# Kernel optimization log

Measured on AMD Instinct MI355X. Metric: run time of the kernel, lower is better.

## Reference

```python
import jax, jax.numpy as jnp
import numpy as np

ALPHA = 2.0      # spikingjelly surrogate.ATan default alpha
TAU_LIF = 2.0    # LIFNode tau
V_TH = 1.0       # spike threshold (v_reset = 0.0, hard reset)


@jax.custom_vjp
def spike_fn(x):
    # Heaviside forward (spikingjelly: x >= 0 -> 1)
    return (x >= 0.0).astype(x.dtype)

def _spike_fwd(x):
    return spike_fn(x), x

def _spike_bwd(x, g):
    # ATan surrogate gradient: alpha/2 / (1 + (pi/2 * alpha * x)^2)
    return (g * (ALPHA / 2.0) / (1.0 + (jnp.pi / 2.0 * ALPHA * x) ** 2),)

spike_fn.defvjp(_spike_fwd, _spike_bwd)


def setup_inputs() -> dict:
    key = jax.random.key(0)
    ks = jax.random.split(key, 5)
    B, T, I, H, O = 256, 1000, 700, 64, 20
    x = jax.random.normal(ks[0], (B, T, I), dtype=jnp.float32)
    W_h = jax.random.normal(ks[1], (H, I), dtype=jnp.float32) / np.sqrt(I).astype(np.float32)
    b_h = jnp.zeros((H,), dtype=jnp.float32)
    W_r = jax.random.normal(ks[2], (O, H), dtype=jnp.float32) / np.sqrt(H).astype(np.float32)
    b_r = jnp.zeros((O,), dtype=jnp.float32)
    tau_m = jax.random.uniform(ks[3], (O,), dtype=jnp.float32, minval=0.0, maxval=4.0)
    return {"x": x, "W_h": W_h, "b_h": b_h, "W_r": W_r, "b_r": b_r, "tau_m": tau_m}


def reference(x, W_h, b_h, W_r, b_r, tau_m):
    B, T, I = x.shape
    H = W_h.shape[0]
    O = W_r.shape[0]
    # One big GEMM for all hidden input currents: [T, B, H]
    currents = jnp.einsum('bti,hi->tbh', x, W_h) + b_h
    beta = jax.nn.sigmoid(tau_m)  # readout leak [O]
    # original accumulates softmax only for t > 10
    mask = (jnp.arange(T) > 10).astype(x.dtype)

    def step(carry, inp):
        v, v_ro, acc = carry
        cur, m = inp
        # LIF charge (decay_input=True, v_reset=0): v += (cur - v)/tau
        v = v + (cur - v) / TAU_LIF
        s = spike_fn(v - V_TH)
        # hard reset to v_reset = 0
        v = v * (1.0 - s)
        # readout leaky integrator
        ro_in = s @ W_r.T + b_r                      # [B, O]
        v_ro = v_ro * beta + (1.0 - beta) * ro_in
        acc = acc + m * jax.nn.softmax(v_ro, axis=-1)
        return (v, v_ro, acc), None

    init = (jnp.zeros((B, H), x.dtype),
            jnp.zeros((B, O), x.dtype),
            jnp.zeros((B, O), x.dtype))
    (_, _, acc), _ = jax.lax.scan(step, init, (currents, mask))
    return acc
```

## Files before the change

kernel.cpp:

```cpp
#include <hip/hip_runtime.h>


typedef float  f32x4  __attribute__((ext_vector_type(4)));
typedef short  short8 __attribute__((ext_vector_type(8)));
typedef unsigned long long ull;

#define B_   256
#define T_   1000
#define K_   700
#define H_   64
#define O_   20
#define NKT  22
#define NCH  200
#define TCH  5
#define TCL  100
#define NCL  10
#define BIL  40

#define OFF_WFRAG  ((size_t)0)
#define OFF_CUR    ((size_t)262144)
#define OFF_MASK   ((size_t)65798144)

__global__ void wprep(const float* __restrict__ Wh, unsigned short* __restrict__ wfrag) {
    int e = blockIdx.x * 256 + threadIdx.x;
    int kt   = e >> 8;
    int rem  = e & 255;
    int nf   = rem >> 6;
    int lane = rem & 63;
    int h     = nf * 16 + (lane & 15);
    int kbase = kt * 32 + ((lane >> 4) & 3) * 8;
    unsigned short* dh = wfrag + (size_t)kt * 4096 + (nf * 64 + lane) * 8;
    unsigned short* dl = dh + 2048;
#pragma unroll
    for (int j = 0; j < 8; ++j) {
        int k = kbase + j;
        float v = (k < K_) ? Wh[(size_t)h * K_ + k] : 0.0f;
        unsigned u  = __builtin_bit_cast(unsigned, v);
        float    fh = __builtin_bit_cast(float, u & 0xffff0000u);
        float    r  = v - fh;
        dh[j] = (unsigned short)(u >> 16);
        dl[j] = (unsigned short)(__builtin_bit_cast(unsigned, r) >> 16);
    }
}

__device__ __forceinline__ void glds16(const void* src, void* lds) {
    __builtin_amdgcn_global_load_lds(
        (const __attribute__((address_space(1))) void*)src,
        (__attribute__((address_space(3))) void*)lds, 16, 0, 0);
}

__device__ __forceinline__ void splitpair(f32x4 p0, f32x4 p1, short8& hi, short8& lo) {
#pragma unroll
    for (int j = 0; j < 4; ++j) {
        {
            unsigned u  = __builtin_bit_cast(unsigned, p0[j]);
            float    fh = __builtin_bit_cast(float, u & 0xffff0000u);
            float    r  = p0[j] - fh;
            hi[j] = (short)(u >> 16);
            lo[j] = (short)(__builtin_bit_cast(unsigned, r) >> 16);
        }
        {
            unsigned u  = __builtin_bit_cast(unsigned, p1[j]);
            float    fh = __builtin_bit_cast(float, u & 0xffff0000u);
            float    r  = p1[j] - fh;
            hi[j + 4] = (short)(u >> 16);
            lo[j + 4] = (short)(__builtin_bit_cast(unsigned, r) >> 16);
        }
    }
}

__device__ __forceinline__ void stage_x32(const float* __restrict__ x, size_t row0,
                                          int kt, int lane, int wid, float* sbuf) {
#pragma unroll
    for (int j = 0; j < 4; ++j) {
        int c   = j * 256 + wid * 64 + lane;
        int row = c >> 3;
        int col = c & 7;
        int csw = (col ^ (row & 7)) << 4;
        int kbyte = kt * 128 + csw;
        if (kbyte + 16 > K_ * 4) kbyte = 0;
        const char* src = (const char*)(x + (row0 + row) * (size_t)K_) + kbyte;
        float* dst = sbuf + (size_t)(j * 256 + wid * 64) * 4;
        glds16(src, dst);
    }
}

__device__ __forceinline__ void stage_w32(const unsigned short* __restrict__ wfrag,
                                          int kt, int lane, int wid, unsigned short* sbuf) {
#pragma unroll
    for (int j = 0; j < 2; ++j) {
        int c = j * 256 + wid * 64 + lane;
        int l = c ^ ((c >> 4) & 7);
        const unsigned short* src = wfrag + (size_t)kt * 4096 + l * 8;
        unsigned short* dst = sbuf + (size_t)(j * 256 + wid * 64) * 8;
        glds16(src, dst);
    }
}

__device__ __forceinline__ void compute32(const float* sbx_, const unsigned short* sbw_,
                                          int lane, int wid, f32x4 (&acc)[2][4]) {
    const f32x4*  xb = (const f32x4*)sbx_;
    const short8* wb = (const short8*)sbw_;
    short8 ah[2], al[2];
    int v0 = (lane >> 4) * 2;
#pragma unroll
    for (int i = 0; i < 2; ++i) {
        int r  = wid * 32 + i * 16 + (lane & 15);
        int c0 = r * 8 + (v0 ^ (r & 7));
        int c1 = r * 8 + ((v0 + 1) ^ (r & 7));
        splitpair(xb[c0], xb[c1], ah[i], al[i]);
    }
#pragma unroll
    for (int n = 0; n < 4; ++n) {
        int lh = n * 64 + lane;
        int ph = lh ^ ((lh >> 4) & 7);
        short8 bhf = wb[ph];
        short8 blf = wb[ph + 256];
#pragma unroll
        for (int i = 0; i < 2; ++i) {
            acc[i][n] = __builtin_amdgcn_mfma_f32_16x16x32_bf16(ah[i], bhf, acc[i][n], 0, 0, 0);
            acc[i][n] = __builtin_amdgcn_mfma_f32_16x16x32_bf16(al[i], bhf, acc[i][n], 0, 0, 0);
            acc[i][n] = __builtin_amdgcn_mfma_f32_16x16x32_bf16(ah[i], blf, acc[i][n], 0, 0, 0);
        }
    }
}

__global__ __launch_bounds__(256, 3) void gemm_cur(const float* __restrict__ x,
                                                   const unsigned short* __restrict__ wfrag,
                                                   const float* __restrict__ b_h,
                                                   float* __restrict__ cur) {
    __shared__ float          sbx[2][4096];
    __shared__ unsigned short sbw[2][4096];
    int tid  = threadIdx.x;
    int lane = tid & 63;
    int wid  = tid >> 6;
    size_t row0 = (size_t)blockIdx.x * 128;

    float bh4[4];
#pragma unroll
    for (int n = 0; n < 4; ++n) bh4[n] = b_h[n * 16 + (lane & 15)];

    f32x4 acc[2][4];
#pragma unroll
    for (int i = 0; i < 2; ++i)
#pragma unroll
        for (int n = 0; n < 4; ++n) acc[i][n] = (f32x4){0.f, 0.f, 0.f, 0.f};

    stage_x32(x, row0, 0, lane, wid, sbx[0]);  stage_w32(wfrag, 0, lane, wid, sbw[0]);
    stage_x32(x, row0, 1, lane, wid, sbx[1]);  stage_w32(wfrag, 1, lane, wid, sbw[1]);

#define GSTEP(T, N)                                                          \
    {                                                                        \
        asm volatile("s_waitcnt vmcnt(" #N ")" ::: "memory");                \
        __builtin_amdgcn_s_barrier();                                        \
        compute32(sbx[(T) & 1], sbw[(T) & 1], lane, wid, acc);               \
        asm volatile("s_waitcnt lgkmcnt(0)" ::: "memory");                   \
        __builtin_amdgcn_s_barrier();                                        \
        if ((T) + 2 < NKT) {                                                 \
            stage_x32(x, row0, (T) + 2, lane, wid, sbx[(T) & 1]);            \
            stage_w32(wfrag, (T) + 2, lane, wid, sbw[(T) & 1]);              \
        }                                                                    \
    }
    GSTEP(0, 6)   GSTEP(1, 6)   GSTEP(2, 6)   GSTEP(3, 6)   GSTEP(4, 6)
    GSTEP(5, 6)   GSTEP(6, 6)   GSTEP(7, 6)   GSTEP(8, 6)   GSTEP(9, 6)
    GSTEP(10, 6)  GSTEP(11, 6)  GSTEP(12, 6)  GSTEP(13, 6)  GSTEP(14, 6)
    GSTEP(15, 6)  GSTEP(16, 6)  GSTEP(17, 6)  GSTEP(18, 6)  GSTEP(19, 6)
    GSTEP(20, 6)  GSTEP(21, 0)
#undef GSTEP

    f32x4* cur4 = (f32x4*)cur;
#pragma unroll
    for (int i = 0; i < 2; ++i) {
        size_t r4 = row0 + wid * 32 + i * 16 + ((lane >> 4) & 3) * 4;
#pragma unroll
        for (int n = 0; n < 4; ++n) {
            f32x4 q;
#pragma unroll
            for (int j = 0; j < 4; ++j) q[j] = acc[i][n][j] + bh4[n];
            cur4[(r4 >> 2) * 64 + n * 16 + (lane & 15)] = q;
        }
    }
}

__global__ __launch_bounds__(64) void lif(const float* __restrict__ cur, ull* __restrict__ masks) {
    int b = blockIdx.x & 255;
    int c = blockIdx.x >> 8;
    int h = threadIdx.x;
    int t0 = c * TCL;
    int ts = (c == 0) ? 0 : (t0 - BIL);
    const f32x4* p = (const f32x4*)cur + (((size_t)b * T_ + ts) >> 2) * 64 + h;
    float v = 0.0f;
    int ngb = (t0 - ts) >> 2;
    for (int g = 0; g < ngb; ++g) {
        f32x4 q = p[g * 64];
#pragma unroll
        for (int j = 0; j < 4; ++j) {
            v = (v + q[j]) * 0.5f;
            v = (v >= 1.0f) ? 0.0f : v;
        }
    }
    p += (size_t)ngb * 64;
    ull* mp = masks + (size_t)b * T_ + t0;
#pragma unroll 2
    for (int g = 0; g < TCL / 4; ++g) {
        f32x4 q = p[g * 64];
#pragma unroll
        for (int j = 0; j < 4; ++j) {
            v = (v + q[j]) * 0.5f;
            bool s = (v >= 1.0f);
            ull m = __ballot(s);
            if (h == 0) mp[g * 4 + j] = m;
            v = s ? 0.0f : v;
        }
    }
}

__global__ __launch_bounds__(512) void readout(const ull* __restrict__ masks,
                                               const float* __restrict__ Wr,
                                               const float* __restrict__ br,
                                               const float* __restrict__ tau,
                                               float* __restrict__ out) {
    __shared__ __align__(16) float wt[64][20];
    __shared__ ull  smask[T_];
    __shared__ __align__(16) float E[NCH][20];
    __shared__ __align__(16) float Sv[NCH][20];
    __shared__ __align__(16) float pacc[NCH][20];
    __shared__ __align__(16) float sScale[20], sBase[20], sBeta[20];
    __shared__ float Pg[8][20], Sst[8][20], part[8][20];

    int tid = threadIdx.x;
    int b   = blockIdx.x;
    for (int i = tid; i < 1280; i += 512) wt[i & 63][i >> 6] = Wr[(size_t)(i >> 6) * 64 + (i & 63)];
    for (int i = tid; i < T_; i += 512) smask[i] = masks[(size_t)b * T_ + i];
    if (tid < 20) {
        float beta = 1.0f / (1.0f + __expf(-tau[tid]));
        sBeta[tid]  = beta;
        sScale[tid] = 1.0f - beta;
        sBase[tid]  = br[tid];
    }
    __syncthreads();

    for (int it = tid; it < NCH * 5; it += 512) {
        int o4 = it % 5;
        int c  = it / 5;
        f32x4 beta4  = *(const f32x4*)&sBeta[o4 * 4];
        f32x4 scale4 = *(const f32x4*)&sScale[o4 * 4];
        f32x4 base4  = *(const f32x4*)&sBase[o4 * 4];
        f32x4 v = {0.f, 0.f, 0.f, 0.f};
        const ull* mp = smask + c * TCH;
#pragma unroll
        for (int j = 0; j < TCH; ++j) {
            ull m = mp[j];
            f32x4 a = {0.f, 0.f, 0.f, 0.f};
            while (m) {
                int h = __builtin_ctzll(m);
                m &= (m - 1);
                a += *(const f32x4*)&wt[h][o4 * 4];
            }
            f32x4 q;
#pragma unroll
            for (int jj = 0; jj < 4; ++jj) q[jj] = scale4[jj] * (base4[jj] + a[jj]);
            v = beta4 * v + q;
        }
        *(f32x4*)&E[c][o4 * 4] = v;
    }
    __syncthreads();

    if (tid < 160) {
        int o = tid >> 3, g = tid & 7;
        float beta = sBeta[o];
        float b2 = beta * beta;
        float bp = b2 * b2 * beta;
        float P = 0.0f;
        for (int c = g * 25; c < g * 25 + 25; ++c) P = bp * P + E[c][o];
        Pg[g][o] = P;
    }
    __syncthreads();

    if (tid < 20) {
        int o = tid;
        float beta = sBeta[o];
        float b2 = beta * beta;
        float bp = b2 * b2 * beta;
        float bp25 = 1.0f;
#pragma unroll
        for (int i = 0; i < 25; ++i) bp25 *= bp;
        float s = 0.0f;
        for (int g = 0; g < 8; ++g) { Sst[g][o] = s; s = bp25 * s + Pg[g][o]; }
    }
    __syncthreads();

    if (tid < 160) {
        int o = tid >> 3, g = tid & 7;
        float beta = sBeta[o];
        float b2 = beta * beta;
        float bp = b2 * b2 * beta;
        float s = Sst[g][o];
        for (int c = g * 25; c < g * 25 + 25; ++c) { Sv[c][o] = s; s = bp * s + E[c][o]; }
    }
    __syncthreads();

    if (tid < NCH) {
        int c = tid;
        float beta[20], v[20], acc[20];
#pragma unroll
        for (int o = 0; o < 20; ++o) {
            beta[o] = sBeta[o];
            v[o]   = Sv[c][o];
            acc[o] = 0.0f;
        }
        int t0 = c * TCH;
        const ull* mp = smask + t0;
#pragma unroll
        for (int j = 0; j < TCH; ++j) {
            int t = t0 + j;
            ull m = mp[j];
            f32x4 a[5];
#pragma unroll
            for (int i = 0; i < 5; ++i) a[i] = (f32x4){0.f, 0.f, 0.f, 0.f};
            while (m) {
                int h = __builtin_ctzll(m);
                m &= (m - 1);
                const f32x4* w4 = (const f32x4*)&wt[h][0];
#pragma unroll
                for (int i = 0; i < 5; ++i) a[i] += w4[i];
            }
#pragma unroll
            for (int o = 0; o < 20; ++o) {
                float q = sScale[o] * (sBase[o] + a[o >> 2][o & 3]);
                v[o] = beta[o] * v[o] + q;
            }
            if (t >= 11) {
                float mx = v[0];
#pragma unroll
                for (int o = 1; o < 20; ++o) mx = fmaxf(mx, v[o]);
                float e[20], ssum = 0.0f;
#pragma unroll
                for (int o = 0; o < 20; ++o) { e[o] = __expf(v[o] - mx); ssum += e[o]; }
                float inv = 1.0f / ssum;
#pragma unroll
                for (int o = 0; o < 20; ++o) acc[o] += e[o] * inv;
            }
        }
#pragma unroll
        for (int o = 0; o < 20; ++o) pacc[c][o] = acc[o];
    }
    __syncthreads();

    if (tid < 160) {
        int o = tid >> 3, g = tid & 7;
        float s = 0.0f;
        for (int c = g * 25; c < g * 25 + 25; ++c) s += pacc[c][o];
        part[g][o] = s;
    }
    __syncthreads();
    if (tid < 20) {
        float s = 0.0f;
#pragma unroll
        for (int g = 0; g < 8; ++g) s += part[g][tid];
        out[(size_t)b * 20 + tid] = s;
    }
}

extern "C" void kernel_launch(void* const* d_in, const int* in_sizes, int n_in,
                              void* d_out, int out_size, void* d_ws, size_t ws_size,
                              hipStream_t stream) {
    const float* x   = (const float*)d_in[0];
    const float* W_h = (const float*)d_in[1];
    const float* b_h = (const float*)d_in[2];
    const float* W_r = (const float*)d_in[3];
    const float* b_r = (const float*)d_in[4];
    const float* tau = (const float*)d_in[5];

    char* ws = (char*)d_ws;
    unsigned short* wfrag = (unsigned short*)(ws + OFF_WFRAG);
    float* cur  = (float*)(ws + OFF_CUR);
    ull*   msk  = (ull*)(ws + OFF_MASK);
    float* out  = (float*)d_out;

    wprep<<<22, 256, 0, stream>>>(W_h, wfrag);
    gemm_cur<<<2000, 256, 0, stream>>>(x, wfrag, b_h, cur);
    lif<<<NCL * 256, 64, 0, stream>>>(cur, msk);
    readout<<<256, 512, 0, stream>>>(msk, W_r, b_r, tau, out);
}
```

Baseline: 218.3 us.

## Retile current GEMM to 64-row blocks with 64-wide K steps

The input-current GEMM now uses 64-row blocks with a K tile of 64 instead of 128 rows with K 32, which halves the number of pipeline steps and doubles the grid to 4000 blocks. The W fragment layout in wprep is reorganised to hold two K sub-fragments per tile, and the LDS weight buffer doubles in size. This cuts barrier and sync overhead per K element and gives more blocks to spread across CUs. In exchange, W is reused across fewer rows per block, so W staging traffic rises, and occupancy is hinted down to 2 blocks per CU. The wprep launch stays at 22 blocks, and its new indexing now spans 11 K tiles.

```diff
diff --git a/kernel.cpp b/kernel.cpp
--- a/kernel.cpp
+++ b/kernel.cpp
@@ -10,7 +10,7 @@
 #define K_   700
 #define H_   64
 #define O_   20
-#define NKT  22
+#define NKT  11
 #define NCH  200
 #define TCH  5
 #define TCL  100
@@ -23,14 +23,16 @@
 
 __global__ void wprep(const float* __restrict__ Wh, unsigned short* __restrict__ wfrag) {
     int e = blockIdx.x * 256 + threadIdx.x;
-    int kt   = e >> 8;
-    int rem  = e & 255;
-    int nf   = rem >> 6;
+    int kt   = e >> 9;
+    int rem  = e & 511;
+    int nf   = rem >> 7;
+    int kf   = (rem >> 6) & 1;
     int lane = rem & 63;
     int h     = nf * 16 + (lane & 15);
-    int kbase = kt * 32 + ((lane >> 4) & 3) * 8;
-    unsigned short* dh = wfrag + (size_t)kt * 4096 + (nf * 64 + lane) * 8;
-    unsigned short* dl = dh + 2048;
+    int kbase = kt * 64 + kf * 32 + ((lane >> 4) & 3) * 8;
+    int slot  = (nf * 2 + kf) * 64 + lane;
+    unsigned short* dh = wfrag + (size_t)kt * 8192 + slot * 8;
+    unsigned short* dl = dh + 4096;
 #pragma unroll
     for (int j = 0; j < 8; ++j) {
         int k = kbase + j;
@@ -69,116 +71,107 @@
     }
 }
 
-__device__ __forceinline__ void stage_x32(const float* __restrict__ x, size_t row0,
-                                          int kt, int lane, int wid, float* sbuf) {
+__device__ __forceinline__ void stage_x64(const float* __restrict__ x, size_t row0,
+                                          int kt, int tid, float* sbuf) {
 #pragma unroll
     for (int j = 0; j < 4; ++j) {
-        int c   = j * 256 + wid * 64 + lane;
-        int row = c >> 3;
-        int col = c & 7;
-        int csw = (col ^ (row & 7)) << 4;
-        int kbyte = kt * 128 + csw;
+        int id = j * 256 + tid;
+        int s  = id >> 9;
+        int r  = (id >> 3) & 63;
+        int pc = id & 7;
+        int c  = pc ^ (r & 7);
+        int kbyte = kt * 256 + s * 128 + (c << 4);
         if (kbyte + 16 > K_ * 4) kbyte = 0;
-        const char* src = (const char*)(x + (row0 + row) * (size_t)K_) + kbyte;
-        float* dst = sbuf + (size_t)(j * 256 + wid * 64) * 4;
+        const char* src = (const char*)(x + (row0 + r) * (size_t)K_) + kbyte;
+        float* dst = sbuf + (size_t)(id & ~63) * 4;
         glds16(src, dst);
     }
 }
 
-__device__ __forceinline__ void stage_w32(const unsigned short* __restrict__ wfrag,
-                                          int kt, int lane, int wid, unsigned short* sbuf) {
-#pragma unroll
-    for (int j = 0; j < 2; ++j) {
-        int c = j * 256 + wid * 64 + lane;
-        int l = c ^ ((c >> 4) & 7);
-        const unsigned short* src = wfrag + (size_t)kt * 4096 + l * 8;
-        unsigned short* dst = sbuf + (size_t)(j * 256 + wid * 64) * 8;
+__device__ __forceinline__ void stage_w64(const unsigned short* __restrict__ wfrag,
+                                          int kt, int tid, unsigned short* sbuf) {
+#pragma unroll
+    for (int j = 0; j < 4; ++j) {
+        int id = j * 256 + tid;
+        const unsigned short* src = wfrag + (size_t)kt * 8192 + id * 8;
+        unsigned short* dst = sbuf + (size_t)(id & ~63) * 8;
         glds16(src, dst);
     }
 }
 
-__device__ __forceinline__ void compute32(const float* sbx_, const unsigned short* sbw_,
-                                          int lane, int wid, f32x4 (&acc)[2][4]) {
-    const f32x4*  xb = (const f32x4*)sbx_;
+__device__ __forceinline__ void compute64(const float* sbx_, const unsigned short* sbw_,
+                                          int lane, int wid, f32x4 (&acc)[4]) {
+    const char*   xb = (const char*)sbx_;
     const short8* wb = (const short8*)sbw_;
-    short8 ah[2], al[2];
-    int v0 = (lane >> 4) * 2;
-#pragma unroll
-    for (int i = 0; i < 2; ++i) {
-        int r  = wid * 32 + i * 16 + (lane & 15);
-        int c0 = r * 8 + (v0 ^ (r & 7));
-        int c1 = r * 8 + ((v0 + 1) ^ (r & 7));
-        splitpair(xb[c0], xb[c1], ah[i], al[i]);
-    }
-#pragma unroll
-    for (int n = 0; n < 4; ++n) {
-        int lh = n * 64 + lane;
-        int ph = lh ^ ((lh >> 4) & 7);
-        short8 bhf = wb[ph];
-        short8 blf = wb[ph + 256];
-#pragma unroll
-        for (int i = 0; i < 2; ++i) {
-            acc[i][n] = __builtin_amdgcn_mfma_f32_16x16x32_bf16(ah[i], bhf, acc[i][n], 0, 0, 0);
-            acc[i][n] = __builtin_amdgcn_mfma_f32_16x16x32_bf16(al[i], bhf, acc[i][n], 0, 0, 0);
-            acc[i][n] = __builtin_amdgcn_mfma_f32_16x16x32_bf16(ah[i], blf, acc[i][n], 0, 0, 0);
-        }
-    }
-}
-
-__global__ __launch_bounds__(256, 3) void gemm_cur(const float* __restrict__ x,
+    int rloc = wid * 16 + (lane & 15);
+    int g2   = ((lane >> 4) & 3) * 2;
+#pragma unroll
+    for (int kf = 0; kf < 2; ++kf) {
+        const char* base = xb + kf * 8192 + rloc * 128;
+        int c0 = g2 ^ (rloc & 7);
+        int c1 = (g2 + 1) ^ (rloc & 7);
+        f32x4 p0 = *(const f32x4*)(base + c0 * 16);
+        f32x4 p1 = *(const f32x4*)(base + c1 * 16);
+        short8 ah, al;
+        splitpair(p0, p1, ah, al);
+#pragma unroll
+        for (int n = 0; n < 4; ++n) {
+            short8 bhf = wb[(n * 2 + kf) * 64 + lane];
+            short8 blf = wb[(n * 2 + kf) * 64 + lane + 512];
+            acc[n] = __builtin_amdgcn_mfma_f32_16x16x32_bf16(ah, bhf, acc[n], 0, 0, 0);
+            acc[n] = __builtin_amdgcn_mfma_f32_16x16x32_bf16(al, bhf, acc[n], 0, 0, 0);
+            acc[n] = __builtin_amdgcn_mfma_f32_16x16x32_bf16(ah, blf, acc[n], 0, 0, 0);
+        }
+    }
+}
+
+__global__ __launch_bounds__(256, 2) void gemm_cur(const float* __restrict__ x,
                                                    const unsigned short* __restrict__ wfrag,
                                                    const float* __restrict__ b_h,
                                                    float* __restrict__ cur) {
     __shared__ float          sbx[2][4096];
-    __shared__ unsigned short sbw[2][4096];
+    __shared__ unsigned short sbw[2][8192];
     int tid  = threadIdx.x;
     int lane = tid & 63;
     int wid  = tid >> 6;
-    size_t row0 = (size_t)blockIdx.x * 128;
+    size_t row0 = (size_t)blockIdx.x * 64;
 
     float bh4[4];
 #pragma unroll
     for (int n = 0; n < 4; ++n) bh4[n] = b_h[n * 16 + (lane & 15)];
 
-    f32x4 acc[2][4];
-#pragma unroll
-    for (int i = 0; i < 2; ++i)
-#pragma unroll
-        for (int n = 0; n < 4; ++n) acc[i][n] = (f32x4){0.f, 0.f, 0.f, 0.f};
-
-    stage_x32(x, row0, 0, lane, wid, sbx[0]);  stage_w32(wfrag, 0, lane, wid, sbw[0]);
-    stage_x32(x, row0, 1, lane, wid, sbx[1]);  stage_w32(wfrag, 1, lane, wid, sbw[1]);
+    f32x4 acc[4];
+#pragma unroll
+    for (int n = 0; n < 4; ++n) acc[n] = (f32x4){0.f, 0.f, 0.f, 0.f};
+
+    stage_x64(x, row0, 0, tid, sbx[0]);  stage_w64(wfrag, 0, tid, sbw[0]);
+    stage_x64(x, row0, 1, tid, sbx[1]);  stage_w64(wfrag, 1, tid, sbw[1]);
 
 #define GSTEP(T, N)                                                          \
     {                                                                        \
         asm volatile("s_waitcnt vmcnt(" #N ")" ::: "memory");                \
         __builtin_amdgcn_s_barrier();                                        \
-        compute32(sbx[(T) & 1], sbw[(T) & 1], lane, wid, acc);               \
+        compute64(sbx[(T) & 1], sbw[(T) & 1], lane, wid, acc);               \
         asm volatile("s_waitcnt lgkmcnt(0)" ::: "memory");                   \
         __builtin_amdgcn_s_barrier();                                        \
         if ((T) + 2 < NKT) {                                                 \
-            stage_x32(x, row0, (T) + 2, lane, wid, sbx[(T) & 1]);            \
-            stage_w32(wfrag, (T) + 2, lane, wid, sbw[(T) & 1]);              \
+            stage_x64(x, row0, (T) + 2, tid, sbx[(T) & 1]);                  \
+            stage_w64(wfrag, (T) + 2, tid, sbw[(T) & 1]);                    \
         }                                                                    \
     }
-    GSTEP(0, 6)   GSTEP(1, 6)   GSTEP(2, 6)   GSTEP(3, 6)   GSTEP(4, 6)
-    GSTEP(5, 6)   GSTEP(6, 6)   GSTEP(7, 6)   GSTEP(8, 6)   GSTEP(9, 6)
-    GSTEP(10, 6)  GSTEP(11, 6)  GSTEP(12, 6)  GSTEP(13, 6)  GSTEP(14, 6)
-    GSTEP(15, 6)  GSTEP(16, 6)  GSTEP(17, 6)  GSTEP(18, 6)  GSTEP(19, 6)
-    GSTEP(20, 6)  GSTEP(21, 0)
+    GSTEP(0, 8)   GSTEP(1, 8)   GSTEP(2, 8)   GSTEP(3, 8)   GSTEP(4, 8)
+    GSTEP(5, 8)   GSTEP(6, 8)   GSTEP(7, 8)   GSTEP(8, 8)   GSTEP(9, 8)
+    GSTEP(10, 0)
 #undef GSTEP
 
     f32x4* cur4 = (f32x4*)cur;
-#pragma unroll
-    for (int i = 0; i < 2; ++i) {
-        size_t r4 = row0 + wid * 32 + i * 16 + ((lane >> 4) & 3) * 4;
-#pragma unroll
-        for (int n = 0; n < 4; ++n) {
-            f32x4 q;
-#pragma unroll
-            for (int j = 0; j < 4; ++j) q[j] = acc[i][n][j] + bh4[n];
-            cur4[(r4 >> 2) * 64 + n * 16 + (lane & 15)] = q;
-        }
+    size_t r4 = row0 + wid * 16 + ((lane >> 4) & 3) * 4;
+#pragma unroll
+    for (int n = 0; n < 4; ++n) {
+        f32x4 q;
+#pragma unroll
+        for (int j = 0; j < 4; ++j) q[j] = acc[n][j] + bh4[n];
+        cur4[(r4 >> 2) * 64 + n * 16 + (lane & 15)] = q;
     }
 }
 
@@ -379,7 +372,7 @@
     float* out  = (float*)d_out;
 
     wprep<<<22, 256, 0, stream>>>(W_h, wfrag);
-    gemm_cur<<<2000, 256, 0, stream>>>(x, wfrag, b_h, cur);
+    gemm_cur<<<4000, 256, 0, stream>>>(x, wfrag, b_h, cur);
     lif<<<NCL * 256, 64, 0, stream>>>(cur, msk);
     readout<<<256, 512, 0, stream>>>(msk, W_r, b_r, tau, out);
 }
```

Result: no change. 222.1 us (+1.8%).

## Keep W_h fragments in registers and repartition GEMM warps by output column

Applied to the files above, without the earlier changes.

The current GEMM now loads every bf16 hi/lo weight fragment for all 22 K-tiles into registers once per block, which removes the per-step weight staging through LDS. Work is repartitioned so each wave owns 16 hidden columns across all 128 rows, rather than 32 rows across all 64 columns. Each wave now splits all 128 x rows into hi/lo bf16 itself, so the split work is done four times per block instead of once. LDS usage is halved and occupancy is raised to 4, in exchange for much higher register pressure (44 short8 weight vectors plus 8 accumulators) and redundant conversion work.

```diff
diff --git a/kernel.cpp b/kernel.cpp
--- a/kernel.cpp
+++ b/kernel.cpp
@@ -70,115 +70,85 @@
 }
 
 __device__ __forceinline__ void stage_x32(const float* __restrict__ x, size_t row0,
-                                          int kt, int lane, int wid, float* sbuf) {
+                                          int kt, int tid, float* sbuf) {
 #pragma unroll
     for (int j = 0; j < 4; ++j) {
-        int c   = j * 256 + wid * 64 + lane;
+        int c   = j * 256 + tid;
         int row = c >> 3;
         int col = c & 7;
         int csw = (col ^ (row & 7)) << 4;
         int kbyte = kt * 128 + csw;
         if (kbyte + 16 > K_ * 4) kbyte = 0;
         const char* src = (const char*)(x + (row0 + row) * (size_t)K_) + kbyte;
-        float* dst = sbuf + (size_t)(j * 256 + wid * 64) * 4;
+        float* dst = sbuf + (size_t)(c & ~63) * 4;
         glds16(src, dst);
     }
 }
 
-__device__ __forceinline__ void stage_w32(const unsigned short* __restrict__ wfrag,
-                                          int kt, int lane, int wid, unsigned short* sbuf) {
-#pragma unroll
-    for (int j = 0; j < 2; ++j) {
-        int c = j * 256 + wid * 64 + lane;
-        int l = c ^ ((c >> 4) & 7);
-        const unsigned short* src = wfrag + (size_t)kt * 4096 + l * 8;
-        unsigned short* dst = sbuf + (size_t)(j * 256 + wid * 64) * 8;
-        glds16(src, dst);
-    }
-}
-
-__device__ __forceinline__ void compute32(const float* sbx_, const unsigned short* sbw_,
-                                          int lane, int wid, f32x4 (&acc)[2][4]) {
-    const f32x4*  xb = (const f32x4*)sbx_;
-    const short8* wb = (const short8*)sbw_;
-    short8 ah[2], al[2];
-    int v0 = (lane >> 4) * 2;
-#pragma unroll
-    for (int i = 0; i < 2; ++i) {
-        int r  = wid * 32 + i * 16 + (lane & 15);
-        int c0 = r * 8 + (v0 ^ (r & 7));
-        int c1 = r * 8 + ((v0 + 1) ^ (r & 7));
-        splitpair(xb[c0], xb[c1], ah[i], al[i]);
-    }
-#pragma unroll
-    for (int n = 0; n < 4; ++n) {
-        int lh = n * 64 + lane;
-        int ph = lh ^ ((lh >> 4) & 7);
-        short8 bhf = wb[ph];
-        short8 blf = wb[ph + 256];
-#pragma unroll
-        for (int i = 0; i < 2; ++i) {
-            acc[i][n] = __builtin_amdgcn_mfma_f32_16x16x32_bf16(ah[i], bhf, acc[i][n], 0, 0, 0);
-            acc[i][n] = __builtin_amdgcn_mfma_f32_16x16x32_bf16(al[i], bhf, acc[i][n], 0, 0, 0);
-            acc[i][n] = __builtin_amdgcn_mfma_f32_16x16x32_bf16(ah[i], blf, acc[i][n], 0, 0, 0);
-        }
-    }
-}
-
-__global__ __launch_bounds__(256, 3) void gemm_cur(const float* __restrict__ x,
+__global__ __launch_bounds__(256, 4) void gemm_cur(const float* __restrict__ x,
                                                    const unsigned short* __restrict__ wfrag,
                                                    const float* __restrict__ b_h,
                                                    float* __restrict__ cur) {
-    __shared__ float          sbx[2][4096];
-    __shared__ unsigned short sbw[2][4096];
+    __shared__ float sbx[2][4096];
     int tid  = threadIdx.x;
     int lane = tid & 63;
     int wid  = tid >> 6;
     size_t row0 = (size_t)blockIdx.x * 128;
 
-    float bh4[4];
-#pragma unroll
-    for (int n = 0; n < 4; ++n) bh4[n] = b_h[n * 16 + (lane & 15)];
-
-    f32x4 acc[2][4];
-#pragma unroll
-    for (int i = 0; i < 2; ++i)
-#pragma unroll
-        for (int n = 0; n < 4; ++n) acc[i][n] = (f32x4){0.f, 0.f, 0.f, 0.f};
-
-    stage_x32(x, row0, 0, lane, wid, sbx[0]);  stage_w32(wfrag, 0, lane, wid, sbw[0]);
-    stage_x32(x, row0, 1, lane, wid, sbx[1]);  stage_w32(wfrag, 1, lane, wid, sbw[1]);
-
-#define GSTEP(T, N)                                                          \
+    short8 wHi[22], wLo[22];
+#pragma unroll
+    for (int kt = 0; kt < 22; ++kt) {
+        const short8* base = (const short8*)(wfrag + (size_t)kt * 4096);
+        wHi[kt] = base[wid * 64 + lane];
+        wLo[kt] = base[256 + wid * 64 + lane];
+    }
+    float bh = b_h[wid * 16 + (lane & 15)];
+
+    f32x4 acc[8];
+#pragma unroll
+    for (int i = 0; i < 8; ++i) acc[i] = (f32x4){0.f, 0.f, 0.f, 0.f};
+
+    stage_x32(x, row0, 0, tid, sbx[0]);
+    stage_x32(x, row0, 1, tid, sbx[1]);
+
+    int g2 = ((lane >> 4) & 3) * 2;
+
+#define GSTEP(KT, N)                                                         \
     {                                                                        \
         asm volatile("s_waitcnt vmcnt(" #N ")" ::: "memory");                \
         __builtin_amdgcn_s_barrier();                                        \
-        compute32(sbx[(T) & 1], sbw[(T) & 1], lane, wid, acc);               \
+        const f32x4* xb = (const f32x4*)sbx[(KT) & 1];                       \
+        short8 bhf = wHi[KT], blf = wLo[KT];                                 \
+        _Pragma("unroll")                                                    \
+        for (int i = 0; i < 8; ++i) {                                        \
+            int r  = i * 16 + (lane & 15);                                   \
+            int c0 = r * 8 + (g2 ^ (r & 7));                                 \
+            int c1 = r * 8 + ((g2 + 1) ^ (r & 7));                           \
+            short8 ah, al;                                                   \
+            splitpair(xb[c0], xb[c1], ah, al);                               \
+            acc[i] = __builtin_amdgcn_mfma_f32_16x16x32_bf16(ah, bhf, acc[i], 0, 0, 0); \
+            acc[i] = __builtin_amdgcn_mfma_f32_16x16x32_bf16(al, bhf, acc[i], 0, 0, 0); \
+            acc[i] = __builtin_amdgcn_mfma_f32_16x16x32_bf16(ah, blf, acc[i], 0, 0, 0); \
+        }                                                                    \
         asm volatile("s_waitcnt lgkmcnt(0)" ::: "memory");                   \
         __builtin_amdgcn_s_barrier();                                        \
-        if ((T) + 2 < NKT) {                                                 \
-            stage_x32(x, row0, (T) + 2, lane, wid, sbx[(T) & 1]);            \
-            stage_w32(wfrag, (T) + 2, lane, wid, sbw[(T) & 1]);              \
-        }                                                                    \
-    }
-    GSTEP(0, 6)   GSTEP(1, 6)   GSTEP(2, 6)   GSTEP(3, 6)   GSTEP(4, 6)
-    GSTEP(5, 6)   GSTEP(6, 6)   GSTEP(7, 6)   GSTEP(8, 6)   GSTEP(9, 6)
-    GSTEP(10, 6)  GSTEP(11, 6)  GSTEP(12, 6)  GSTEP(13, 6)  GSTEP(14, 6)
-    GSTEP(15, 6)  GSTEP(16, 6)  GSTEP(17, 6)  GSTEP(18, 6)  GSTEP(19, 6)
-    GSTEP(20, 6)  GSTEP(21, 0)
+        if ((KT) + 2 < NKT) stage_x32(x, row0, (KT) + 2, tid, sbx[(KT) & 1]); \
+    }
+    GSTEP(0, 4)   GSTEP(1, 4)   GSTEP(2, 4)   GSTEP(3, 4)   GSTEP(4, 4)
+    GSTEP(5, 4)   GSTEP(6, 4)   GSTEP(7, 4)   GSTEP(8, 4)   GSTEP(9, 4)
+    GSTEP(10, 4)  GSTEP(11, 4)  GSTEP(12, 4)  GSTEP(13, 4)  GSTEP(14, 4)
+    GSTEP(15, 4)  GSTEP(16, 4)  GSTEP(17, 4)  GSTEP(18, 4)  GSTEP(19, 4)
+    GSTEP(20, 4)  GSTEP(21, 0)
 #undef GSTEP
 
     f32x4* cur4 = (f32x4*)cur;
 #pragma unroll
-    for (int i = 0; i < 2; ++i) {
-        size_t r4 = row0 + wid * 32 + i * 16 + ((lane >> 4) & 3) * 4;
-#pragma unroll
-        for (int n = 0; n < 4; ++n) {
-            f32x4 q;
-#pragma unroll
-            for (int j = 0; j < 4; ++j) q[j] = acc[i][n][j] + bh4[n];
-            cur4[(r4 >> 2) * 64 + n * 16 + (lane & 15)] = q;
-        }
+    for (int i = 0; i < 8; ++i) {
+        size_t r4 = row0 + i * 16 + ((lane >> 4) & 3) * 4;
+        f32x4 q;
+#pragma unroll
+        for (int j = 0; j < 4; ++j) q[j] = acc[i][j] + bh;
+        cur4[(r4 >> 2) * 64 + wid * 16 + (lane & 15)] = q;
     }
 }
 
```

New measurement: 329.0 us. +50.8%, slower.
